# Kernel optimization log

Measured on AMD Instinct MI355X. Metric: run time of the kernel, lower is better.

The kernel has to match this reference:

```python
import jax, jax.numpy as jnp
import numpy as np

C, S, H = 64, 2048, 512
ITERATIONS = 3

def squash(x, eps=1e-07):
    # per-vector squash along last dim: (|x|^2/(1+|x|^2)) * x/|x|
    sq = jnp.sum(x * x, axis=-1, keepdims=True)
    safe_norm = jnp.sqrt(sq + eps)
    scale = sq / (1.0 + sq)
    return scale * (x / safe_norm)

def setup_inputs() -> dict:
    key = jax.random.key(0)
    k1, k2 = jax.random.split(key)
    x = jax.random.normal(k1, (C * S, H), dtype=jnp.float32)
    # xavier-normal init for Linear(H, H)
    std = np.sqrt(2.0 / (H + H)).astype(np.float32)
    W_weight = jax.random.normal(k2, (H, H), dtype=jnp.float32) * std
    W_bias = jnp.zeros((H,), dtype=jnp.float32)
    return {"x": x, "W_weight": W_weight, "W_bias": W_bias}

def reference(x, W_weight, W_bias):
    xr = x.reshape(C, S, H)
    # e_ij = squash(Linear(x))  -> [C, S, H]
    e_ij = squash(jnp.einsum('csh,oh->cso', xr, W_weight) + W_bias)
    b_ij = jnp.zeros((C, S), dtype=x.dtype)
    c_i = jnp.zeros((C, H), dtype=x.dtype)
    for _ in range(ITERATIONS):
        d_i = jax.nn.softmax(b_ij, axis=1)[..., None]          # [C, S, 1]
        c_i = squash(jnp.sum(d_i * e_ij, axis=1))              # [C, H]
        b_ij = b_ij + jnp.einsum('csh,ch->cs', e_ij, c_i)      # [C, S]
    return c_i
```

## Files before the change

### kernel.cpp

```cpp
#include <hip/hip_runtime.h>
#include <hip/hip_fp16.h>

#define HDIM 512

typedef __fp16 fp16x2 __attribute__((ext_vector_type(2)));
typedef _Float16 h8 __attribute__((ext_vector_type(8)));
typedef __attribute__((ext_vector_type(4))) float floatx4;

__device__ __forceinline__ void lds_barrier() {
  asm volatile("s_waitcnt lgkmcnt(0)\n\ts_barrier" ::: "memory");
}
__device__ __forceinline__ void issue_fence() {
  asm volatile("" ::: "memory");
}

__global__ __launch_bounds__(256) void prep_w_kernel(
    const float* __restrict__ W, _Float16* __restrict__ wf) {
  int i = (blockIdx.x * 256 + threadIdx.x) * 4;
  float4 f = *(const float4*)(W + i);
  wf[i + 0] = (_Float16)f.x;
  wf[i + 1] = (_Float16)f.y;
  wf[i + 2] = (_Float16)f.z;
  wf[i + 3] = (_Float16)f.w;
}

#define XS_H (128 * 40)
#define WS_H (512 * 32)

__device__ __forceinline__ void issue_w_dma(const _Float16* __restrict__ wf,
                                            _Float16* dst, int kt, int tid,
                                            int widx) {
#pragma unroll
  for (int q = 0; q < 4; ++q) {
    int idx = q * 512 + tid;
    int n = idx >> 2;
    int src = (idx & 3) ^ ((n >> 1) & 3);
    size_t goff = (size_t)n * HDIM + kt * 32 + src * 8;
    __builtin_amdgcn_global_load_lds(
        (const __attribute__((address_space(1))) void*)(wf + goff),
        (__attribute__((address_space(3))) void*)(dst +
                                                  (q * 512 + widx * 64) * 8),
        16, 0, 0);
  }
}

__global__ __launch_bounds__(512, 2) void gemm_kernel(
    const float* __restrict__ x, const _Float16* __restrict__ wf,
    const float* __restrict__ bias, __half* __restrict__ e,
    float* __restrict__ u_gemm) {
  __shared__ __align__(16) _Float16 smem[2 * XS_H + 4 * WS_H];
  _Float16* xs[2] = {smem, smem + XS_H};
  _Float16* wsm = smem + 2 * XS_H;

  const int tid = threadIdx.x;
  const int lane = tid & 63;
  const int widx = tid >> 6;
  const int wave_m = widx >> 2;
  const int wave_n = widx & 3;
  const int lrow = lane & 15, quad = lane >> 4;

  const int bid = blockIdx.x;
  const int row0 = bid * 128;

  const int xrow = tid >> 2;
  const int xcg = tid & 3;
  const float* xbase = x + (size_t)(row0 + xrow) * HDIM + xcg * 8;

  floatx4 acc[4][8];
#pragma unroll
  for (int i = 0; i < 4; ++i)
#pragma unroll
    for (int j = 0; j < 8; ++j) acc[i][j] = (floatx4){0.f, 0.f, 0.f, 0.f};

  float4 xr[2][2];

  issue_w_dma(wf, wsm + 0 * WS_H, 0, tid, widx);
  issue_fence();
  xr[0][0] = *(const float4*)xbase;
  xr[0][1] = *(const float4*)(xbase + 4);
  issue_fence();
  issue_w_dma(wf, wsm + 1 * WS_H, 1, tid, widx);
  issue_fence();
  xr[1][0] = *(const float4*)(xbase + 32);
  xr[1][1] = *(const float4*)(xbase + 36);
  issue_fence();

  const int chunkB = quad ^ ((lrow >> 1) & 3);

#pragma unroll
  for (int t = 0; t < 16; ++t) {
    {
      float4 a0 = xr[t & 1][0], a1 = xr[t & 1][1];
      union { h8 v8; fp16x2 v2[4]; } u;
      u.v2[0] = __builtin_amdgcn_cvt_pkrtz(a0.x, a0.y);
      u.v2[1] = __builtin_amdgcn_cvt_pkrtz(a0.z, a0.w);
      u.v2[2] = __builtin_amdgcn_cvt_pkrtz(a1.x, a1.y);
      u.v2[3] = __builtin_amdgcn_cvt_pkrtz(a1.z, a1.w);
      *(h8*)&xs[t & 1][xrow * 40 + xcg * 8] = u.v8;
    }
    if (t <= 13) {
      issue_w_dma(wf, wsm + ((t + 2) & 3) * WS_H, t + 2, tid, widx);
      issue_fence();
      const float* gp = xbase + (t + 2) * 32;
      xr[t & 1][0] = *(const float4*)gp;
      xr[t & 1][1] = *(const float4*)(gp + 4);
      issue_fence();
    }
    lds_barrier();
    const _Float16* xsr = xs[t & 1];
    const _Float16* wcur = wsm + (t & 3) * WS_H;
    h8 a[4], bh[8];
#pragma unroll
    for (int mt = 0; mt < 4; ++mt)
      a[mt] = *(const h8*)&xsr[(wave_m * 64 + mt * 16 + lrow) * 40 + quad * 8];
#pragma unroll
    for (int nt = 0; nt < 8; ++nt)
      bh[nt] =
          *(const h8*)&wcur[(wave_n * 128 + nt * 16 + lrow) * 32 + chunkB * 8];
    __builtin_amdgcn_s_setprio(1);
#pragma unroll
    for (int mt = 0; mt < 4; ++mt)
#pragma unroll
      for (int nt = 0; nt < 8; ++nt)
        acc[mt][nt] = __builtin_amdgcn_mfma_f32_16x16x32_f16(
            a[mt], bh[nt], acc[mt][nt], 0, 0, 0);
    __builtin_amdgcn_s_setprio(0);
  }

  float* sqp = (float*)smem;
  float* scs = (float*)smem + 512;
  float* upl = (float*)smem + 640;

  float bias_v[8];
  int colg[8];
#pragma unroll
  for (int nt = 0; nt < 8; ++nt) {
    colg[nt] = wave_n * 128 + nt * 16 + lrow;
    bias_v[nt] = bias[colg[nt]];
  }
#pragma unroll
  for (int mt = 0; mt < 4; ++mt) {
#pragma unroll
    for (int r = 0; r < 4; ++r) {
      float s = 0.f;
#pragma unroll
      for (int nt = 0; nt < 8; ++nt) {
        float yv = acc[mt][nt][r] + bias_v[nt];
        s += yv * yv;
      }
      s += __shfl_xor(s, 1, 64);
      s += __shfl_xor(s, 2, 64);
      s += __shfl_xor(s, 4, 64);
      s += __shfl_xor(s, 8, 64);
      if (lrow == 0)
        sqp[wave_n * 128 + wave_m * 64 + mt * 16 + quad * 4 + r] = s;
    }
  }
  lds_barrier();
  if (tid < 128) {
    float s = sqp[tid] + sqp[128 + tid] + sqp[256 + tid] + sqp[384 + tid];
    scs[tid] = s / ((1.f + s) * sqrtf(s + 1e-7f));
  }
  lds_barrier();

  float up[8] = {0.f, 0.f, 0.f, 0.f, 0.f, 0.f, 0.f, 0.f};
#pragma unroll
  for (int mt = 0; mt < 4; ++mt) {
#pragma unroll
    for (int r = 0; r < 4; ++r) {
      int row_local = wave_m * 64 + mt * 16 + quad * 4 + r;
      float scv = scs[row_local];
      __half* erow = e + (size_t)(row0 + row_local) * HDIM;
#pragma unroll
      for (int nt = 0; nt < 8; ++nt) {
        float ev = (acc[mt][nt][r] + bias_v[nt]) * scv;
        erow[colg[nt]] = __float2half(ev);
        up[nt] += ev;
      }
    }
  }
#pragma unroll
  for (int nt = 0; nt < 8; ++nt) {
    float v = up[nt];
    v += __shfl_xor(v, 16, 64);
    v += __shfl_xor(v, 32, 64);
    if (quad == 0) upl[wave_m * 512 + colg[nt]] = v;
  }
  lds_barrier();
  u_gemm[(size_t)(bid >> 4) * 16 * HDIM + (size_t)(bid & 15) * HDIM + tid] =
      upl[tid] + upl[512 + tid];
}

template <bool FIRST>
__global__ __launch_bounds__(256, 4) void route_iter_kernel(
    const __half* __restrict__ e, const float* __restrict__ u_in,
    const float* __restrict__ den_in, float* __restrict__ b,
    float* __restrict__ u_out, float* __restrict__ den_out) {
  const int tid = threadIdx.x;
  const int w = tid >> 6;
  const int lane = tid & 63;
  const int bid = blockIdx.x;
  const int cap = bid >> 4;
  const int r0 = bid * 128;

  __shared__ float csh[512];
  __shared__ float red[256];
  __shared__ float lred[4][512];
  __shared__ float ldn[4];
  __shared__ float sden;

  float v0 = 0.f, v1 = 0.f;
  {
    const float* upb = u_in + (size_t)cap * 16 * HDIM;
#pragma unroll
    for (int ch = 0; ch < 16; ++ch) {
      v0 += upb[ch * HDIM + tid];
      v1 += upb[ch * HDIM + tid + 256];
    }
  }
  float den;
  if (FIRST) {
    den = 2048.f;
  } else {
    red[tid] = (tid < 16) ? den_in[cap * 16 + tid] : 0.f;
    __syncthreads();
    if (tid == 0) {
      float s = 0.f;
#pragma unroll
      for (int i = 0; i < 16; ++i) s += red[i];
      sden = s;
    }
    __syncthreads();
    den = sden;
    __syncthreads();
  }
  v0 /= den;
  v1 /= den;
  red[tid] = v0 * v0 + v1 * v1;
  __syncthreads();
  for (int s = 128; s > 0; s >>= 1) {
    if (tid < s) red[tid] += red[tid + s];
    __syncthreads();
  }
  const float sqv = red[0];
  const float scv = sqv / ((1.f + sqv) * sqrtf(sqv + 1e-7f));
  csh[tid] = v0 * scv;
  csh[tid + 256] = v1 * scv;
  __syncthreads();

  float c8[8];
#pragma unroll
  for (int k = 0; k < 8; ++k) c8[k] = csh[lane * 8 + k];
  float u8[8] = {0, 0, 0, 0, 0, 0, 0, 0};
  float den_w = 0.f;

  union U { int4 v; __half hh[8]; };
  U cur[4], nxt[4];
  const __half* yb = e + (size_t)(r0 + w * 32) * HDIM + lane * 8;
#pragma unroll
  for (int j = 0; j < 4; ++j) cur[j].v = *(const int4*)(yb + (size_t)j * HDIM);

  for (int g = 0; g < 8; ++g) {
    if (g < 7) {
#pragma unroll
      for (int j = 0; j < 4; ++j)
        nxt[j].v = *(const int4*)(yb + (size_t)(g * 4 + 4 + j) * HDIM);
    }
    float dot[4];
#pragma unroll
    for (int j = 0; j < 4; ++j) {
      float d = 0.f;
#pragma unroll
      for (int k = 0; k < 8; ++k) d += __half2float(cur[j].hh[k]) * c8[k];
      dot[j] = d;
    }
#pragma unroll
    for (int s = 1; s < 64; s <<= 1) {
#pragma unroll
      for (int j = 0; j < 4; ++j) dot[j] += __shfl_xor(dot[j], s, 64);
    }
#pragma unroll
    for (int j = 0; j < 4; ++j) {
      const int rl = w * 32 + g * 4 + j;
      float bn = FIRST ? dot[j] : (b[r0 + rl] + dot[j]);
      if (FIRST && lane == 0) b[r0 + rl] = bn;
      float wj = __expf(bn);
      den_w += wj;
#pragma unroll
      for (int k = 0; k < 8; ++k) u8[k] += wj * __half2float(cur[j].hh[k]);
    }
#pragma unroll
    for (int j = 0; j < 4; ++j) cur[j] = nxt[j];
  }

#pragma unroll
  for (int k = 0; k < 8; ++k) lred[w][lane * 8 + k] = u8[k];
  if (lane == 0) ldn[w] = den_w;
  __syncthreads();
  float* ur = u_out + (size_t)cap * 16 * HDIM + (size_t)(bid & 15) * HDIM;
#pragma unroll
  for (int hh = 0; hh < 2; ++hh) {
    int h = hh * 256 + tid;
    ur[h] = lred[0][h] + lred[1][h] + lred[2][h] + lred[3][h];
  }
  if (tid == 0)
    den_out[cap * 16 + (bid & 15)] = ldn[0] + ldn[1] + ldn[2] + ldn[3];
}

__global__ __launch_bounds__(512) void route_final_kernel(
    const float* __restrict__ u_in, const float* __restrict__ den_in,
    float* __restrict__ out) {
  const int cap = blockIdx.x;
  const int t = threadIdx.x;
  __shared__ float red[512];
  __shared__ float sden;

  red[t] = (t < 16) ? den_in[cap * 16 + t] : 0.f;
  __syncthreads();
  if (t == 0) {
    float s = 0.f;
#pragma unroll
    for (int i = 0; i < 16; ++i) s += red[i];
    sden = s;
  }
  __syncthreads();
  const float den = sden;

  float v = 0.f;
  const float* up = u_in + (size_t)cap * 16 * HDIM + t;
#pragma unroll
  for (int ch = 0; ch < 16; ++ch) v += up[ch * HDIM];
  v /= den;

  __syncthreads();
  red[t] = v * v;
  __syncthreads();
  for (int s = 256; s > 0; s >>= 1) {
    if (t < s) red[t] += red[t + s];
    __syncthreads();
  }
  const float sqv = red[0];
  const float scv = sqv / ((1.f + sqv) * sqrtf(sqv + 1e-7f));
  out[cap * HDIM + t] = v * scv;
}

extern "C" void kernel_launch(void* const* d_in, const int* in_sizes, int n_in,
                              void* d_out, int out_size, void* d_ws,
                              size_t ws_size, hipStream_t stream) {
  const float* x = (const float*)d_in[0];
  const float* W = (const float*)d_in[1];
  const float* bias = (const float*)d_in[2];
  float* out = (float*)d_out;
  char* ws = (char*)d_ws;

  __half* e = (__half*)ws;
  float* u_gemm = (float*)(ws + (size_t)134217728);
  float* u_a = u_gemm + (size_t)64 * 16 * 512;
  float* u_b = u_a + (size_t)64 * 16 * 512;
  float* den_a = u_b + (size_t)64 * 16 * 512;
  float* den_b = den_a + 1024;
  float* b = den_b + 1024;
  _Float16* wf = (_Float16*)(b + 131072);

  prep_w_kernel<<<256, 256, 0, stream>>>(W, wf);
  gemm_kernel<<<1024, 512, 0, stream>>>(x, wf, bias, e, u_gemm);

  route_iter_kernel<true><<<1024, 256, 0, stream>>>(e, u_gemm, nullptr, b,
                                                    u_a, den_a);
  route_iter_kernel<false><<<1024, 256, 0, stream>>>(e, u_a, den_a, b,
                                                     u_b, den_b);
  route_final_kernel<<<64, 512, 0, stream>>>(u_b, den_b, out);
}
```

Baseline: 469.9 us.

## Halve GEMM row tile to 64, double-buffer W, raise occupancy and route grid

The GEMM block tile shrinks from 128 to 64 rows, with each of the 8 waves covering a 64-column slice. The W staging buffer drops from four to two stages, with explicit vmcnt waits, and the kernel launch bound rises to 4 blocks per CU. The smaller LDS footprint and register count are meant to raise occupancy and double the grid to 2048 blocks for better CU balance. Routing kernels likewise process 64 rows per block with 32 partials per capsule. The cost is that every W tile is now loaded for only 64 rows, doubling W traffic, and the partial-sum reductions grow larger.

Result: slower. 686.3 us (+46.1%).

```diff
diff --git a/kernel.cpp b/kernel.cpp
--- a/kernel.cpp
+++ b/kernel.cpp
@@ -4,6 +4,7 @@
 #define HDIM 512
 
 typedef __fp16 fp16x2 __attribute__((ext_vector_type(2)));
+typedef _Float16 h4 __attribute__((ext_vector_type(4)));
 typedef _Float16 h8 __attribute__((ext_vector_type(8)));
 typedef __attribute__((ext_vector_type(4))) float floatx4;
 
@@ -24,65 +25,59 @@
   wf[i + 3] = (_Float16)f.w;
 }
 
-#define XS_H (128 * 40)
+#define XS_H (64 * 40)
 #define WS_H (512 * 32)
 
 __device__ __forceinline__ void issue_w_dma(const _Float16* __restrict__ wf,
-                                            _Float16* dst, int kt, int tid,
+                                            _Float16* dst, int kt, int lane,
                                             int widx) {
 #pragma unroll
   for (int q = 0; q < 4; ++q) {
-    int idx = q * 512 + tid;
-    int n = idx >> 2;
-    int src = (idx & 3) ^ ((n >> 1) & 3);
-    size_t goff = (size_t)n * HDIM + kt * 32 + src * 8;
+    int src = (lane & 3) ^ ((lane >> 3) & 3);
+    int row = widx * 64 + q * 16 + (lane >> 2);
+    size_t goff = (size_t)row * HDIM + kt * 32 + src * 8;
     __builtin_amdgcn_global_load_lds(
         (const __attribute__((address_space(1))) void*)(wf + goff),
-        (__attribute__((address_space(3))) void*)(dst +
-                                                  (q * 512 + widx * 64) * 8),
+        (__attribute__((address_space(3))) void*)(
+            dst + (widx * 64 + q * 16) * 32),
         16, 0, 0);
   }
 }
 
-__global__ __launch_bounds__(512, 2) void gemm_kernel(
+__global__ __launch_bounds__(512, 4) void gemm_kernel(
     const float* __restrict__ x, const _Float16* __restrict__ wf,
     const float* __restrict__ bias, __half* __restrict__ e,
     float* __restrict__ u_gemm) {
-  __shared__ __align__(16) _Float16 smem[2 * XS_H + 4 * WS_H];
-  _Float16* xs[2] = {smem, smem + XS_H};
+  __shared__ __align__(16) _Float16 smem[2 * XS_H + 2 * WS_H];
+  _Float16* xs0 = smem;
+  _Float16* xs1 = smem + XS_H;
   _Float16* wsm = smem + 2 * XS_H;
 
   const int tid = threadIdx.x;
   const int lane = tid & 63;
   const int widx = tid >> 6;
-  const int wave_m = widx >> 2;
-  const int wave_n = widx & 3;
   const int lrow = lane & 15, quad = lane >> 4;
 
   const int bid = blockIdx.x;
-  const int row0 = bid * 128;
-
-  const int xrow = tid >> 2;
-  const int xcg = tid & 3;
-  const float* xbase = x + (size_t)(row0 + xrow) * HDIM + xcg * 8;
-
-  floatx4 acc[4][8];
+  const int row0 = bid * 64;
+
+  const int xrow = tid >> 3;
+  const int xcg = tid & 7;
+  const float* xbase = x + (size_t)(row0 + xrow) * HDIM + xcg * 4;
+
+  floatx4 acc[4][4];
 #pragma unroll
   for (int i = 0; i < 4; ++i)
 #pragma unroll
-    for (int j = 0; j < 8; ++j) acc[i][j] = (floatx4){0.f, 0.f, 0.f, 0.f};
-
-  float4 xr[2][2];
-
-  issue_w_dma(wf, wsm + 0 * WS_H, 0, tid, widx);
+    for (int j = 0; j < 4; ++j) acc[i][j] = (floatx4){0.f, 0.f, 0.f, 0.f};
+
+  float4 xr[2];
+
+  issue_w_dma(wf, wsm, 0, lane, widx);
   issue_fence();
-  xr[0][0] = *(const float4*)xbase;
-  xr[0][1] = *(const float4*)(xbase + 4);
+  xr[0] = *(const float4*)xbase;
   issue_fence();
-  issue_w_dma(wf, wsm + 1 * WS_H, 1, tid, widx);
-  issue_fence();
-  xr[1][0] = *(const float4*)(xbase + 32);
-  xr[1][1] = *(const float4*)(xbase + 36);
+  xr[1] = *(const float4*)(xbase + 32);
   issue_fence();
 
   const int chunkB = quad ^ ((lrow >> 1) & 3);
@@ -90,38 +85,40 @@
 #pragma unroll
   for (int t = 0; t < 16; ++t) {
     {
-      float4 a0 = xr[t & 1][0], a1 = xr[t & 1][1];
-      union { h8 v8; fp16x2 v2[4]; } u;
+      float4 a0 = xr[t & 1];
+      union { h4 v4; fp16x2 v2[2]; } u;
       u.v2[0] = __builtin_amdgcn_cvt_pkrtz(a0.x, a0.y);
       u.v2[1] = __builtin_amdgcn_cvt_pkrtz(a0.z, a0.w);
-      u.v2[2] = __builtin_amdgcn_cvt_pkrtz(a1.x, a1.y);
-      u.v2[3] = __builtin_amdgcn_cvt_pkrtz(a1.z, a1.w);
-      *(h8*)&xs[t & 1][xrow * 40 + xcg * 8] = u.v8;
+      _Float16* xsd = (t & 1) ? xs1 : xs0;
+      *(h4*)&xsd[xrow * 40 + xcg * 4] = u.v4;
+    }
+    lds_barrier();
+    if (t <= 14) {
+      issue_w_dma(wf, wsm + ((t + 1) & 1) * WS_H, t + 1, lane, widx);
+      issue_fence();
     }
     if (t <= 13) {
-      issue_w_dma(wf, wsm + ((t + 2) & 3) * WS_H, t + 2, tid, widx);
+      xr[t & 1] = *(const float4*)(xbase + (t + 2) * 32);
       issue_fence();
-      const float* gp = xbase + (t + 2) * 32;
-      xr[t & 1][0] = *(const float4*)gp;
-      xr[t & 1][1] = *(const float4*)(gp + 4);
-      issue_fence();
-    }
-    lds_barrier();
-    const _Float16* xsr = xs[t & 1];
-    const _Float16* wcur = wsm + (t & 3) * WS_H;
-    h8 a[4], bh[8];
+    }
+    if (t >= 1 && t <= 13) asm volatile("s_waitcnt vmcnt(6)" ::: "memory");
+    else if (t == 14) asm volatile("s_waitcnt vmcnt(5)" ::: "memory");
+    else if (t == 15) asm volatile("s_waitcnt vmcnt(0)" ::: "memory");
+    const _Float16* xsr = (t & 1) ? xs1 : xs0;
+    const _Float16* wcur = wsm + (t & 1) * WS_H;
+    h8 a[4], bh[4];
 #pragma unroll
     for (int mt = 0; mt < 4; ++mt)
-      a[mt] = *(const h8*)&xsr[(wave_m * 64 + mt * 16 + lrow) * 40 + quad * 8];
-#pragma unroll
-    for (int nt = 0; nt < 8; ++nt)
-      bh[nt] =
-          *(const h8*)&wcur[(wave_n * 128 + nt * 16 + lrow) * 32 + chunkB * 8];
+      a[mt] = *(const h8*)&xsr[(mt * 16 + lrow) * 40 + quad * 8];
+#pragma unroll
+    for (int nt = 0; nt < 4; ++nt)
+      bh[nt] = *(const h8*)&wcur[(widx * 64 + nt * 16 + lrow) * 32 +
+                                 chunkB * 8];
     __builtin_amdgcn_s_setprio(1);
 #pragma unroll
     for (int mt = 0; mt < 4; ++mt)
 #pragma unroll
-      for (int nt = 0; nt < 8; ++nt)
+      for (int nt = 0; nt < 4; ++nt)
         acc[mt][nt] = __builtin_amdgcn_mfma_f32_16x16x32_f16(
             a[mt], bh[nt], acc[mt][nt], 0, 0, 0);
     __builtin_amdgcn_s_setprio(0);
@@ -129,14 +126,13 @@
 
   float* sqp = (float*)smem;
   float* scs = (float*)smem + 512;
-  float* upl = (float*)smem + 640;
-
-  float bias_v[8];
-  int colg[8];
-#pragma unroll
-  for (int nt = 0; nt < 8; ++nt) {
-    colg[nt] = wave_n * 128 + nt * 16 + lrow;
-    bias_v[nt] = bias[colg[nt]];
+
+  float bias_v[4];
+  int coll[4];
+#pragma unroll
+  for (int nt = 0; nt < 4; ++nt) {
+    coll[nt] = widx * 64 + nt * 16 + lrow;
+    bias_v[nt] = bias[coll[nt]];
   }
 #pragma unroll
   for (int mt = 0; mt < 4; ++mt) {
@@ -144,7 +140,7 @@
     for (int r = 0; r < 4; ++r) {
       float s = 0.f;
 #pragma unroll
-      for (int nt = 0; nt < 8; ++nt) {
+      for (int nt = 0; nt < 4; ++nt) {
         float yv = acc[mt][nt][r] + bias_v[nt];
         s += yv * yv;
       }
@@ -152,47 +148,47 @@
       s += __shfl_xor(s, 2, 64);
       s += __shfl_xor(s, 4, 64);
       s += __shfl_xor(s, 8, 64);
-      if (lrow == 0)
-        sqp[wave_n * 128 + wave_m * 64 + mt * 16 + quad * 4 + r] = s;
+      if (lrow == 0) sqp[widx * 64 + mt * 16 + quad * 4 + r] = s;
     }
   }
   lds_barrier();
-  if (tid < 128) {
-    float s = sqp[tid] + sqp[128 + tid] + sqp[256 + tid] + sqp[384 + tid];
+  if (tid < 64) {
+    float s = 0.f;
+#pragma unroll
+    for (int w = 0; w < 8; ++w) s += sqp[w * 64 + tid];
     scs[tid] = s / ((1.f + s) * sqrtf(s + 1e-7f));
   }
   lds_barrier();
 
-  float up[8] = {0.f, 0.f, 0.f, 0.f, 0.f, 0.f, 0.f, 0.f};
+  float up[4] = {0.f, 0.f, 0.f, 0.f};
 #pragma unroll
   for (int mt = 0; mt < 4; ++mt) {
 #pragma unroll
     for (int r = 0; r < 4; ++r) {
-      int row_local = wave_m * 64 + mt * 16 + quad * 4 + r;
-      float scv = scs[row_local];
-      __half* erow = e + (size_t)(row0 + row_local) * HDIM;
-#pragma unroll
-      for (int nt = 0; nt < 8; ++nt) {
+      int rowl = mt * 16 + quad * 4 + r;
+      float scv = scs[rowl];
+      __half* erow = e + (size_t)(row0 + rowl) * HDIM;
+#pragma unroll
+      for (int nt = 0; nt < 4; ++nt) {
         float ev = (acc[mt][nt][r] + bias_v[nt]) * scv;
-        erow[colg[nt]] = __float2half(ev);
+        erow[coll[nt]] = __float2half(ev);
         up[nt] += ev;
       }
     }
   }
 #pragma unroll
-  for (int nt = 0; nt < 8; ++nt) {
+  for (int nt = 0; nt < 4; ++nt) {
     float v = up[nt];
     v += __shfl_xor(v, 16, 64);
     v += __shfl_xor(v, 32, 64);
-    if (quad == 0) upl[wave_m * 512 + colg[nt]] = v;
-  }
-  lds_barrier();
-  u_gemm[(size_t)(bid >> 4) * 16 * HDIM + (size_t)(bid & 15) * HDIM + tid] =
-      upl[tid] + upl[512 + tid];
+    if (quad == 0)
+      u_gemm[(size_t)(bid >> 5) * 32 * HDIM + (size_t)(bid & 31) * HDIM +
+             coll[nt]] = v;
+  }
 }
 
 template <bool FIRST>
-__global__ __launch_bounds__(256, 4) void route_iter_kernel(
+__global__ __launch_bounds__(256, 6) void route_iter_kernel(
     const __half* __restrict__ e, const float* __restrict__ u_in,
     const float* __restrict__ den_in, float* __restrict__ b,
     float* __restrict__ u_out, float* __restrict__ den_out) {
@@ -200,8 +196,8 @@
   const int w = tid >> 6;
   const int lane = tid & 63;
   const int bid = blockIdx.x;
-  const int cap = bid >> 4;
-  const int r0 = bid * 128;
+  const int cap = bid >> 5;
+  const int r0 = bid * 64;
 
   __shared__ float csh[512];
   __shared__ float red[256];
@@ -211,9 +207,9 @@
 
   float v0 = 0.f, v1 = 0.f;
   {
-    const float* upb = u_in + (size_t)cap * 16 * HDIM;
-#pragma unroll
-    for (int ch = 0; ch < 16; ++ch) {
+    const float* upb = u_in + (size_t)cap * 32 * HDIM;
+#pragma unroll
+    for (int ch = 0; ch < 32; ++ch) {
       v0 += upb[ch * HDIM + tid];
       v1 += upb[ch * HDIM + tid + 256];
     }
@@ -222,12 +218,12 @@
   if (FIRST) {
     den = 2048.f;
   } else {
-    red[tid] = (tid < 16) ? den_in[cap * 16 + tid] : 0.f;
+    red[tid] = (tid < 32) ? den_in[cap * 32 + tid] : 0.f;
     __syncthreads();
     if (tid == 0) {
       float s = 0.f;
 #pragma unroll
-      for (int i = 0; i < 16; ++i) s += red[i];
+      for (int i = 0; i < 32; ++i) s += red[i];
       sden = s;
     }
     __syncthreads();
@@ -256,12 +252,12 @@
 
   union U { int4 v; __half hh[8]; };
   U cur[4], nxt[4];
-  const __half* yb = e + (size_t)(r0 + w * 32) * HDIM + lane * 8;
+  const __half* yb = e + (size_t)(r0 + w * 16) * HDIM + lane * 8;
 #pragma unroll
   for (int j = 0; j < 4; ++j) cur[j].v = *(const int4*)(yb + (size_t)j * HDIM);
 
-  for (int g = 0; g < 8; ++g) {
-    if (g < 7) {
+  for (int g = 0; g < 4; ++g) {
+    if (g < 3) {
 #pragma unroll
       for (int j = 0; j < 4; ++j)
         nxt[j].v = *(const int4*)(yb + (size_t)(g * 4 + 4 + j) * HDIM);
@@ -281,7 +277,7 @@
     }
 #pragma unroll
     for (int j = 0; j < 4; ++j) {
-      const int rl = w * 32 + g * 4 + j;
+      const int rl = w * 16 + g * 4 + j;
       float bn = FIRST ? dot[j] : (b[r0 + rl] + dot[j]);
       if (FIRST && lane == 0) b[r0 + rl] = bn;
       float wj = __expf(bn);
@@ -297,14 +293,14 @@
   for (int k = 0; k < 8; ++k) lred[w][lane * 8 + k] = u8[k];
   if (lane == 0) ldn[w] = den_w;
   __syncthreads();
-  float* ur = u_out + (size_t)cap * 16 * HDIM + (size_t)(bid & 15) * HDIM;
+  float* ur = u_out + (size_t)cap * 32 * HDIM + (size_t)(bid & 31) * HDIM;
 #pragma unroll
   for (int hh = 0; hh < 2; ++hh) {
     int h = hh * 256 + tid;
     ur[h] = lred[0][h] + lred[1][h] + lred[2][h] + lred[3][h];
   }
   if (tid == 0)
-    den_out[cap * 16 + (bid & 15)] = ldn[0] + ldn[1] + ldn[2] + ldn[3];
+    den_out[cap * 32 + (bid & 31)] = ldn[0] + ldn[1] + ldn[2] + ldn[3];
 }
 
 __global__ __launch_bounds__(512) void route_final_kernel(
@@ -315,21 +311,21 @@
   __shared__ float red[512];
   __shared__ float sden;
 
-  red[t] = (t < 16) ? den_in[cap * 16 + t] : 0.f;
+  red[t] = (t < 32) ? den_in[cap * 32 + t] : 0.f;
   __syncthreads();
   if (t == 0) {
     float s = 0.f;
 #pragma unroll
-    for (int i = 0; i < 16; ++i) s += red[i];
+    for (int i = 0; i < 32; ++i) s += red[i];
     sden = s;
   }
   __syncthreads();
   const float den = sden;
 
   float v = 0.f;
-  const float* up = u_in + (size_t)cap * 16 * HDIM + t;
-#pragma unroll
-  for (int ch = 0; ch < 16; ++ch) v += up[ch * HDIM];
+  const float* up = u_in + (size_t)cap * 32 * HDIM + t;
+#pragma unroll
+  for (int ch = 0; ch < 32; ++ch) v += up[ch * HDIM];
   v /= den;
 
   __syncthreads();
@@ -355,19 +351,19 @@
 
   __half* e = (__half*)ws;
   float* u_gemm = (float*)(ws + (size_t)134217728);
-  float* u_a = u_gemm + (size_t)64 * 16 * 512;
-  float* u_b = u_a + (size_t)64 * 16 * 512;
-  float* den_a = u_b + (size_t)64 * 16 * 512;
-  float* den_b = den_a + 1024;
-  float* b = den_b + 1024;
+  float* u_a = u_gemm + (size_t)64 * 32 * 512;
+  float* u_b = u_a + (size_t)64 * 32 * 512;
+  float* den_a = u_b + (size_t)64 * 32 * 512;
+  float* den_b = den_a + 2048;
+  float* b = den_b + 2048;
   _Float16* wf = (_Float16*)(b + 131072);
 
   prep_w_kernel<<<256, 256, 0, stream>>>(W, wf);
-  gemm_kernel<<<1024, 512, 0, stream>>>(x, wf, bias, e, u_gemm);
-
-  route_iter_kernel<true><<<1024, 256, 0, stream>>>(e, u_gemm, nullptr, b,
+  gemm_kernel<<<2048, 512, 0, stream>>>(x, wf, bias, e, u_gemm);
+
+  route_iter_kernel<true><<<2048, 256, 0, stream>>>(e, u_gemm, nullptr, b,
                                                     u_a, den_a);
-  route_iter_kernel<false><<<1024, 256, 0, stream>>>(e, u_a, den_a, b,
+  route_iter_kernel<false><<<2048, 256, 0, stream>>>(e, u_a, den_a, b,
                                                      u_b, den_b);
   route_final_kernel<<<64, 512, 0, stream>>>(u_b, den_b, out);
 }
```
